# Performance work log

Hardware: AMD Instinct MI355X
Metric: run time of the kernel (lower is better)

The kernel has to match this reference:

```python
import jax, jax.numpy as jnp
import numpy as np

VOCAB = 32000
WORDVEC = 256
HIDDEN = 512
NULL_TOKEN = 0


def setup_inputs() -> dict:
    key = jax.random.key(0)
    ks = jax.random.split(key, 8)
    N, Tp1 = 16, 257
    captions = jax.random.randint(ks[0], (N, Tp1), 0, VOCAB, dtype=jnp.int64 if jax.config.jax_enable_x64 else jnp.int32)
    W_embed = jax.random.normal(ks[1], (VOCAB, WORDVEC), jnp.float32) / 100.0
    Wx = jax.random.normal(ks[2], (WORDVEC, 4 * HIDDEN), jnp.float32) / np.sqrt(WORDVEC).astype(np.float32)
    Wh = jax.random.normal(ks[3], (HIDDEN, 4 * HIDDEN), jnp.float32) / np.sqrt(HIDDEN).astype(np.float32)
    b = jnp.zeros((4 * HIDDEN,), jnp.float32)
    W_vocab = jax.random.normal(ks[4], (HIDDEN, VOCAB), jnp.float32) / np.sqrt(HIDDEN).astype(np.float32)
    b_vocab = jnp.zeros((VOCAB,), jnp.float32)
    h_init = jax.random.normal(ks[5], (HIDDEN,), jnp.float32)
    return {"captions": captions, "W_embed": W_embed, "Wx": Wx, "Wh": Wh,
            "b": b, "W_vocab": W_vocab, "b_vocab": b_vocab, "h_init": h_init}


def reference(captions, W_embed, Wx, Wh, b, W_vocab, b_vocab, h_init):
    cap_in = captions[:, :-1]   # [N, T]
    cap_out = captions[:, 1:]   # [N, T]
    mask = (cap_out != NULL_TOKEN).astype(jnp.float32)
    N = cap_in.shape[0]
    H = h_init.shape[0]

    # Embedding lookup: [N, T, D]
    x = W_embed[cap_in]
    # Precompute input projections as one big GEMM: [T, N, 4H]
    xw = jnp.einsum('ntd,dk->tnk', x, Wx) + b

    h0 = jnp.tile(h_init, (N, 1))          # [N, H]
    c0 = jnp.zeros_like(h0)                 # lstm_forward starts c at zeros

    def step(carry, a_x):
        h, c = carry
        a = a_x + h @ Wh                    # [N, 4H]
        i, f, o, g = jnp.split(a, 4, axis=-1)
        i = jax.nn.sigmoid(i)
        f = jax.nn.sigmoid(f)
        o = jax.nn.sigmoid(o)
        g = jnp.tanh(g)
        c = f * c + i * g
        h = o * jnp.tanh(c)
        return (h, c), h

    _, hs = jax.lax.scan(step, (h0, c0), xw)  # hs: [T, N, H]

    # Temporal affine: [N, T, V]
    logits = jnp.einsum('tnh,hv->ntv', hs, W_vocab) + b_vocab
    logp = jax.nn.log_softmax(logits, axis=-1)
    nll = -jnp.take_along_axis(logp, cap_out[..., None], axis=-1)[..., 0]
    loss = jnp.sum(nll * mask) / N
    return loss
```

## Files before the change

### kernel.cpp

```cpp
#include <hip/hip_runtime.h>

#define VOCAB   32000
#define WORDVEC 256
#define HIDDEN  512
#define TSTEPS  256
#define NBATCH  16
#define NROWS   (TSTEPS*NBATCH)
#define GATES   (4*HIDDEN)
#define NVB     125
#define NWG     32
#define NVBLK   8000
#define SPINCAP (1<<16)

typedef __attribute__((ext_vector_type(8))) short short8;
typedef __attribute__((ext_vector_type(4))) float f32x4;
typedef unsigned long long u64;

#define AGLOAD(p) __hip_atomic_load((p), __ATOMIC_RELAXED, __HIP_MEMORY_SCOPE_AGENT)

__device__ __forceinline__ unsigned short f2bf(float x){
    union { float f; unsigned int u; } v; v.f = x;
    unsigned int r = v.u + 0x7fffu + ((v.u >> 16) & 1u);
    return (unsigned short)(r >> 16);
}

__global__ __launch_bounds__(256) void prep_all(const int* __restrict__ captions,
        const float* __restrict__ Wemb, const float* __restrict__ Wx,
        const float* __restrict__ b, float* __restrict__ xw,
        const float* __restrict__ Wh, unsigned short* __restrict__ Whp,
        const float* __restrict__ h_init, u64* __restrict__ hx,
        const float* __restrict__ Wv, unsigned short* __restrict__ WvP,
        int* __restrict__ prog){
    __shared__ float s[64][65];
    float (*xs)[WORDVEC] = (float(*)[WORDVEC])s;
    __shared__ int toks[8];
    int bid = blockIdx.x;
    int tid = threadIdx.x;
    if (bid < 512){
        int r0 = bid * 8;
        if (tid < 8){
            int r = r0 + tid; int t = r >> 4, n = r & 15;
            toks[tid] = captions[n*257 + t];
        }
        __syncthreads();
        for (int i = 0; i < 8; ++i){
            int lin = tid + i*256;
            int ri = lin >> 8, d = lin & 255;
            xs[ri][d] = Wemb[(long)toks[ri]*WORDVEC + d];
        }
        __syncthreads();
        float4 b0 = *(const float4*)(b + tid*4);
        float4 b1 = *(const float4*)(b + 1024 + tid*4);
        float acc[8][8];
        for (int ri = 0; ri < 8; ++ri){
            acc[ri][0]=b0.x; acc[ri][1]=b0.y; acc[ri][2]=b0.z; acc[ri][3]=b0.w;
            acc[ri][4]=b1.x; acc[ri][5]=b1.y; acc[ri][6]=b1.z; acc[ri][7]=b1.w;
        }
        for (int d = 0; d < WORDVEC; ++d){
            float4 w0 = *(const float4*)(Wx + (long)d*GATES + tid*4);
            float4 w1 = *(const float4*)(Wx + (long)d*GATES + 1024 + tid*4);
            #pragma unroll
            for (int ri = 0; ri < 8; ++ri){
                float xv = xs[ri][d];
                acc[ri][0] += xv*w0.x; acc[ri][1] += xv*w0.y;
                acc[ri][2] += xv*w0.z; acc[ri][3] += xv*w0.w;
                acc[ri][4] += xv*w1.x; acc[ri][5] += xv*w1.y;
                acc[ri][6] += xv*w1.z; acc[ri][7] += xv*w1.w;
            }
        }
        for (int ri = 0; ri < 8; ++ri){
            float4 o0 = {acc[ri][0],acc[ri][1],acc[ri][2],acc[ri][3]};
            float4 o1 = {acc[ri][4],acc[ri][5],acc[ri][6],acc[ri][7]};
            *(float4*)(xw + (long)(r0+ri)*GATES + tid*4) = o0;
            *(float4*)(xw + (long)(r0+ri)*GATES + 1024 + tid*4) = o1;
        }
    } else if (bid < 544){
        int w = bid - 512;
        for (int item = tid; item < 4096; item += 256){
            int f = item >> 6;
            int L = item & 63;
            int kt = f >> 2, nt = f & 3;
            int q = L >> 4, ln = L & 15;
            int col = nt*HIDDEN + w*16 + ln;
            short8 vvec;
            for (int jj = 0; jj < 8; ++jj){
                int k = kt*32 + q*8 + jj;
                vvec[jj] = (short)f2bf(Wh[(long)k*GATES + col]);
            }
            *(short8*)(Whp + ((long)w*4096 + item)*8) = vvec;
        }
    } else if (bid < 560){
        if (bid == 544 && tid < 32) prog[tid] = 0;
        int p = (bid - 544)*256 + tid;
        int fq = p >> 6;
        int j  = (p & 3) * 2;
        int u0 = (fq>>2)*32 + (fq&3)*8 + j;
        u64 pk = (u64)f2bf(h_init[u0]) | ((u64)f2bf(h_init[u0+1]) << 16);
        hx[p] = pk;
    } else {
        int tile = bid - 560;
        int v0 = (tile >> 3) * 64;
        int k0 = (tile & 7) * 64;
        for (int i = 0; i < 16; ++i){
            int lin = tid + i*256;
            int kk = lin >> 6, vv = lin & 63;
            s[kk][vv] = Wv[(long)(k0+kk)*VOCAB + v0 + vv];
        }
        __syncthreads();
        for (int i = 0; i < 2; ++i){
            int lr = tid + i*256;
            int f  = lr >> 6;
            int vbl = f >> 1, ktl = f & 1;
            int L = lr & 63, q = L >> 4, ln = L & 15;
            short8 o;
            #pragma unroll
            for (int j = 0; j < 8; ++j)
                o[j] = (short)f2bf(s[ktl*32 + q*8 + j][vbl*16 + ln]);
            long vb = (long)(tile >> 3)*4 + vbl;
            long kt = (long)(tile & 7)*2 + ktl;
            *(short8*)(WvP + ((vb*16 + kt)*64 + L)*8) = o;
        }
    }
}

__global__ __launch_bounds__(256, 2) void lstm_vocab(const float* __restrict__ xw,
        const unsigned short* __restrict__ Whp, u64* __restrict__ hx,
        unsigned short* __restrict__ hsP, int* __restrict__ prog,
        const unsigned short* __restrict__ WvP, const float* __restrict__ bvoc,
        const int* __restrict__ captions, float* __restrict__ pmax,
        float* __restrict__ psum, float* __restrict__ tlog){
    __shared__ unsigned int hstage[4096];
    __shared__ float a_s[4][16][16];
    __shared__ int   tgt_s[64];
    __shared__ float wmax_s[4][64], wsum_s[4][64];
    int tid = threadIdx.x;

    if (blockIdx.x >= NWG){
        int vid = blockIdx.x - NWG;
        int pri = vid / 2000;
        int idx = vid % 2000;
        int bn  = idx % 125;
        int bm  = (idx / 125) * 4 + pri;
        int need = (pri + 1) * 4;

        if (tid == 0){
            int cnt = 0;
            for (;;){
                int mn = 1 << 30;
                for (int i = 0; i < 32; ++i){
                    int p = AGLOAD(&prog[i]);
                    mn = p < mn ? p : mn;
                }
                if (mn >= need) break;
                __builtin_amdgcn_s_sleep(32);
                if (++cnt > SPINCAP) break;
            }
        }
        __syncthreads();

        int wv = tid >> 6, L = tid & 63;
        int q = L >> 4, ln = L & 15;
        if (tid < 64){
            int rg = bm*64 + tid;
            tgt_s[tid] = captions[(rg >> 8)*257 + (rg & 255) + 1];
        }
        __syncthreads();
        f32x4 acc[4][4];
        for (int mt=0;mt<4;++mt) for (int nt=0;nt<4;++nt) acc[mt][nt] = (f32x4){0.f,0.f,0.f,0.f};
        int colb = bn*256 + wv*64;
        const unsigned short* aB = hsP + ((long)(bm*4)*16)*512;
        const unsigned short* bB = WvP + ((long)(bn*16 + wv*4)*16)*512;
        #pragma unroll 4
        for (int kt = 0; kt < 16; ++kt){
            short8 a[4], bb[4];
            #pragma unroll
            for (int mt=0;mt<4;++mt)
                a[mt] = *(const short8*)(aB + ((long)(mt*16 + kt)*64 + L)*8);
            #pragma unroll
            for (int nt=0;nt<4;++nt)
                bb[nt] = *(const short8*)(bB + ((long)(nt*16 + kt)*64 + L)*8);
            #pragma unroll
            for (int mt=0;mt<4;++mt)
                #pragma unroll
                for (int nt=0;nt<4;++nt)
                    acc[mt][nt] = __builtin_amdgcn_mfma_f32_16x16x32_bf16(a[mt], bb[nt], acc[mt][nt], 0,0,0);
        }
        float bv[4];
        #pragma unroll
        for (int nt=0;nt<4;++nt) bv[nt] = bvoc[colb + nt*16 + ln];
        #pragma unroll
        for (int mt=0;mt<4;++mt) for (int nt=0;nt<4;++nt) for (int r=0;r<4;++r)
            acc[mt][nt][r] += bv[nt];
        #pragma unroll
        for (int mt=0;mt<4;++mt) for (int r=0;r<4;++r){
            int rl = mt*16 + q*4 + r;
            int tg = tgt_s[rl] - colb;
            if (tg >= 0 && tg < 64){
                int nt = tg >> 4;
                if ((tg & 15) == ln) tlog[bm*64 + rl] = acc[mt][nt][r];
            }
        }
        #pragma unroll
        for (int mt=0;mt<4;++mt){
            #pragma unroll
            for (int r=0;r<4;++r){
                float m = fmaxf(fmaxf(acc[mt][0][r],acc[mt][1][r]), fmaxf(acc[mt][2][r],acc[mt][3][r]));
                for (int d=1; d<16; d<<=1) m = fmaxf(m, __shfl_xor(m, d, 16));
                float s = __expf(acc[mt][0][r]-m) + __expf(acc[mt][1][r]-m)
                        + __expf(acc[mt][2][r]-m) + __expf(acc[mt][3][r]-m);
                for (int d=1; d<16; d<<=1) s += __shfl_xor(s, d, 16);
                if (ln == 0){ int rl = mt*16 + q*4 + r; wmax_s[wv][rl] = m; wsum_s[wv][rl] = s; }
            }
        }
        __syncthreads();
        if (tid < 64){
            float M = fmaxf(fmaxf(wmax_s[0][tid],wmax_s[1][tid]), fmaxf(wmax_s[2][tid],wmax_s[3][tid]));
            float S = 0.f;
            for (int ww=0; ww<4; ++ww) S += wsum_s[ww][tid]*__expf(wmax_s[ww][tid]-M);
            pmax[(long)bn*NROWS + bm*64 + tid] = M;
            psum[(long)bn*NROWS + bm*64 + tid] = S;
        }
        return;
    }

    int w = blockIdx.x;
    int wv = tid >> 6;
    int L = tid & 63;
    int q = L >> 4, ln = L & 15;
    int s_idx = tid >> 4, jl = tid & 15;

    short8 bw[16];
    #pragma unroll
    for (int kt = 0; kt < 16; ++kt)
        bw[kt] = *(const short8*)(Whp + ((long)w*4096 + (kt*4+wv)*64 + L)*8);

    float c_r = 0.f;
    int fq_pub = (w>>1)*4 + (w&1)*2 + (jl>>3);
    int pubIdx = fq_pub*64 + s_idx*4 + ((jl>>1)&3);
    int kt_h = w >> 1;
    int q_h  = ((w & 1) << 1) | (jl >> 3);
    int j_h  = jl & 7;
    unsigned int* hsP32 = (unsigned int*)hsP;

    for (int t = 0; t < TSTEPS; ++t){
        long xb = (long)(t*16 + s_idx)*GATES + w*16 + jl;
        float xg0 = xw[xb], xg1 = xw[xb+512], xg2 = xw[xb+1024], xg3 = xw[xb+1536];

        const u64* hr = hx + (t & 1)*4096;
        u64*       hw = hx + ((t+1) & 1)*4096;

        u64 v[16];
        #pragma unroll
        for (int i = 0; i < 16; ++i)
            v[i] = AGLOAD(hr + tid + i*256);
        for (;;){
            u64 bad = 0;
            #pragma unroll
            for (int i = 0; i < 16; ++i) bad |= (v[i] >> 32) ^ (u64)(unsigned)t;
            if (!bad) break;
            #pragma unroll
            for (int i = 0; i < 16; ++i)
                v[i] = AGLOAD(hr + tid + i*256);
        }
        #pragma unroll
        for (int i = 0; i < 16; ++i) hstage[tid + i*256] = (unsigned)v[i];
        __syncthreads();

        f32x4 acc = {0.f,0.f,0.f,0.f};
        #pragma unroll
        for (int kt = 0; kt < 16; ++kt){
            short8 a = *(const short8*)((const unsigned short*)hstage + (kt*256 + q*64 + ln*4)*2);
            acc = __builtin_amdgcn_mfma_f32_16x16x32_bf16(a, bw[kt], acc, 0, 0, 0);
        }
        #pragma unroll
        for (int r = 0; r < 4; ++r) a_s[wv][q*4 + r][ln] = acc[r];
        __syncthreads();

        float ai = a_s[0][s_idx][jl] + xg0;
        float af = a_s[1][s_idx][jl] + xg1;
        float ao = a_s[2][s_idx][jl] + xg2;
        float ag = a_s[3][s_idx][jl] + xg3;
        float ig = 1.f/(1.f + __expf(-ai));
        float fg = 1.f/(1.f + __expf(-af));
        float og = 1.f/(1.f + __expf(-ao));
        float gg = 2.f/(1.f + __expf(-2.f*ag)) - 1.f;
        c_r = fg*c_r + ig*gg;
        float hv = og * (2.f/(1.f + __expf(-2.f*c_r)) - 1.f);
        unsigned short hb = f2bf(hv);

        int hv32 = (int)hb;
        int other = __shfl(hv32, L ^ 1);
        int rb = s_idx*16 + (t >> 4);
        if ((jl & 1) == 0){
            u64 pk = (u64)(unsigned short)hv32
                   | ((u64)(unsigned short)other << 16)
                   | ((u64)(unsigned)(t+1) << 32);
            __hip_atomic_store(hw + pubIdx, pk, __ATOMIC_RELAXED, __HIP_MEMORY_SCOPE_AGENT);
            unsigned int hp = (unsigned int)(unsigned short)hv32
                            | ((unsigned int)(unsigned short)other << 16);
            __hip_atomic_store(hsP32 + (((long)(rb*16 + kt_h))*64 + q_h*16 + (t & 15))*4 + (j_h >> 1),
                               hp, __ATOMIC_RELAXED, __HIP_MEMORY_SCOPE_AGENT);
        }
        if ((t & 15) == 15){
            asm volatile("s_waitcnt vmcnt(0)" ::: "memory");
            __syncthreads();
            if (tid == 0)
                __hip_atomic_store(&prog[w], (t >> 4) + 1, __ATOMIC_RELAXED, __HIP_MEMORY_SCOPE_AGENT);
        }
    }
}

__global__ __launch_bounds__(256) void reduce_loss(const float* __restrict__ pmax,
        const float* __restrict__ psum, const float* __restrict__ tlog,
        const int* __restrict__ captions, float* __restrict__ out){
    int r = blockIdx.x*256 + threadIdx.x;
    float M = -1e30f;
    for (int p=0;p<NVB;++p) M = fmaxf(M, pmax[(long)p*NROWS + r]);
    float S = 0.f;
    for (int p=0;p<NVB;++p) S += psum[(long)p*NROWS + r]*__expf(pmax[(long)p*NROWS + r]-M);
    float lse = M + logf(S);
    float nll = lse - tlog[r];
    int tok = captions[(r >> 8)*257 + (r & 255) + 1];
    float val = (tok != 0) ? nll : 0.f;
    __shared__ float red[256];
    red[threadIdx.x] = val; __syncthreads();
    for (int s=128; s>0; s>>=1){
        if (threadIdx.x < s) red[threadIdx.x] += red[threadIdx.x+s];
        __syncthreads();
    }
    if (threadIdx.x == 0) atomicAdd(out, red[0] * (1.0f/16.0f));
}

extern "C" void kernel_launch(void* const* d_in, const int* in_sizes, int n_in,
                              void* d_out, int out_size, void* d_ws, size_t ws_size,
                              hipStream_t stream){
    const int*   captions = (const int*)  d_in[0];
    const float* Wemb     = (const float*)d_in[1];
    const float* Wx       = (const float*)d_in[2];
    const float* Wh       = (const float*)d_in[3];
    const float* b        = (const float*)d_in[4];
    const float* Wv       = (const float*)d_in[5];
    const float* bvoc     = (const float*)d_in[6];
    const float* h_init   = (const float*)d_in[7];

    char* ws = (char*)d_ws;
    float*          xw   = (float*)         (ws + 0);
    unsigned short* WvP  = (unsigned short*)(ws + 33554432);
    unsigned short* hsP  = (unsigned short*)(ws + 66322432);
    float*          pmax = (float*)         (ws + 70516736);
    float*          psum = (float*)         (ws + 72564736);
    float*          tlog = (float*)         (ws + 74612736);
    unsigned short* Whp  = (unsigned short*)(ws + 74629120);
    u64*            hx   = (u64*)           (ws + 76726272);
    int*            prog = (int*)           (ws + 76791808);

    float* out_f = (float*)d_out;

    (void)hipMemsetAsync(d_out, 0, sizeof(float), stream);

    hipLaunchKernelGGL(prep_all,    dim3(4560),       dim3(256), 0, stream,
                       captions, Wemb, Wx, b, xw, Wh, Whp, h_init, hx, Wv, WvP, prog);
    hipLaunchKernelGGL(lstm_vocab,  dim3(NWG+NVBLK),  dim3(256), 0, stream,
                       xw, Whp, hx, hsP, prog, WvP, bvoc, captions, pmax, psum, tlog);
    hipLaunchKernelGGL(reduce_loss, dim3(16),         dim3(256), 0, stream,
                       pmax, psum, tlog, captions, out_f);
}
```

Measured before the change: 1.169 ms.

## Restructure vocab GEMM inner loop for register pressure and remap tile order

The vocab-projection blocks now run a non-unrolled k loop that loads A/B fragments in staged groups, separated by scheduling barriers, and reloads two B fragments instead of holding all eight in registers. This lowers register pressure and removes the min-2-waves launch bound. Block-to-tile mapping is also permuted so consecutive blocks cover different column/row tiles, changing L2 reuse of W_vocab. The cost is extra global loads per k step and a new scheduling order that may expose latency.

```diff
diff --git a/kernel.cpp b/kernel.cpp
--- a/kernel.cpp
+++ b/kernel.cpp
@@ -17,6 +17,7 @@
 typedef unsigned long long u64;
 
 #define AGLOAD(p) __hip_atomic_load((p), __ATOMIC_RELAXED, __HIP_MEMORY_SCOPE_AGENT)
+#define MFMA16(a,b,c) __builtin_amdgcn_mfma_f32_16x16x32_bf16((a),(b),(c),0,0,0)
 
 __device__ __forceinline__ unsigned short f2bf(float x){
     union { float f; unsigned int u; } v; v.f = x;
@@ -123,7 +124,7 @@
     }
 }
 
-__global__ __launch_bounds__(256, 2) void lstm_vocab(const float* __restrict__ xw,
+__global__ __launch_bounds__(256) void lstm_vocab(const float* __restrict__ xw,
         const unsigned short* __restrict__ Whp, u64* __restrict__ hx,
         unsigned short* __restrict__ hsP, int* __restrict__ prog,
         const unsigned short* __restrict__ WvP, const float* __restrict__ bvoc,
@@ -139,8 +140,9 @@
         int vid = blockIdx.x - NWG;
         int pri = vid / 2000;
         int idx = vid % 2000;
-        int bn  = idx % 125;
-        int bm  = (idx / 125) * 4 + pri;
+        int p   = (idx & 7)*250 + (idx >> 3);
+        int bn  = p >> 4;
+        int bm  = (p & 15)*4 + pri;
         int need = (pri + 1) * 4;
 
         if (tid == 0){
@@ -148,8 +150,8 @@
             for (;;){
                 int mn = 1 << 30;
                 for (int i = 0; i < 32; ++i){
-                    int p = AGLOAD(&prog[i]);
-                    mn = p < mn ? p : mn;
+                    int pv = AGLOAD(&prog[i]);
+                    mn = pv < mn ? pv : mn;
                 }
                 if (mn >= need) break;
                 __builtin_amdgcn_s_sleep(32);
@@ -168,22 +170,31 @@
         f32x4 acc[4][4];
         for (int mt=0;mt<4;++mt) for (int nt=0;nt<4;++nt) acc[mt][nt] = (f32x4){0.f,0.f,0.f,0.f};
         int colb = bn*256 + wv*64;
-        const unsigned short* aB = hsP + ((long)(bm*4)*16)*512;
-        const unsigned short* bB = WvP + ((long)(bn*16 + wv*4)*16)*512;
-        #pragma unroll 4
+        const unsigned short* aB = hsP + ((long)(bm*4)*16)*512 + (long)L*8;
+        const unsigned short* bB = WvP + ((long)(bn*16 + wv*4)*16)*512 + (long)L*8;
+        #pragma unroll 1
         for (int kt = 0; kt < 16; ++kt){
-            short8 a[4], bb[4];
-            #pragma unroll
-            for (int mt=0;mt<4;++mt)
-                a[mt] = *(const short8*)(aB + ((long)(mt*16 + kt)*64 + L)*8);
-            #pragma unroll
-            for (int nt=0;nt<4;++nt)
-                bb[nt] = *(const short8*)(bB + ((long)(nt*16 + kt)*64 + L)*8);
-            #pragma unroll
-            for (int mt=0;mt<4;++mt)
-                #pragma unroll
-                for (int nt=0;nt<4;++nt)
-                    acc[mt][nt] = __builtin_amdgcn_mfma_f32_16x16x32_bf16(a[mt], bb[nt], acc[mt][nt], 0,0,0);
+            const short8* aK = (const short8*)(aB + (long)kt*512);
+            const short8* bK = (const short8*)(bB + (long)kt*512);
+            short8 a0 = aK[0],    a1 = aK[1024];
+            short8 b0 = bK[0],    b1 = bK[1024];
+            acc[0][0] = MFMA16(a0,b0,acc[0][0]); acc[0][1] = MFMA16(a0,b1,acc[0][1]);
+            acc[1][0] = MFMA16(a1,b0,acc[1][0]); acc[1][1] = MFMA16(a1,b1,acc[1][1]);
+            __builtin_amdgcn_sched_barrier(0);
+            short8 b2 = bK[2048], b3 = bK[3072];
+            acc[0][2] = MFMA16(a0,b2,acc[0][2]); acc[0][3] = MFMA16(a0,b3,acc[0][3]);
+            acc[1][2] = MFMA16(a1,b2,acc[1][2]); acc[1][3] = MFMA16(a1,b3,acc[1][3]);
+            __builtin_amdgcn_sched_barrier(0);
+            short8 a2 = aK[2048], a3 = aK[3072];
+            acc[2][2] = MFMA16(a2,b2,acc[2][2]); acc[2][3] = MFMA16(a2,b3,acc[2][3]);
+            acc[3][2] = MFMA16(a3,b2,acc[3][2]); acc[3][3] = MFMA16(a3,b3,acc[3][3]);
+            __builtin_amdgcn_sched_barrier(0);
+            u64 bKo = (u64)bK; asm volatile("" : "+v"(bKo));
+            const short8* bK2 = (const short8*)bKo;
+            short8 c0 = bK2[0], c1 = bK2[1024];
+            acc[2][0] = MFMA16(a2,c0,acc[2][0]); acc[2][1] = MFMA16(a2,c1,acc[2][1]);
+            acc[3][0] = MFMA16(a3,c0,acc[3][0]); acc[3][1] = MFMA16(a3,c1,acc[3][1]);
+            __builtin_amdgcn_sched_barrier(0);
         }
         float bv[4];
         #pragma unroll
@@ -270,7 +281,7 @@
         #pragma unroll
         for (int kt = 0; kt < 16; ++kt){
             short8 a = *(const short8*)((const unsigned short*)hstage + (kt*256 + q*64 + ln*4)*2);
-            acc = __builtin_amdgcn_mfma_f32_16x16x32_bf16(a, bw[kt], acc, 0, 0, 0);
+            acc = MFMA16(a, bw[kt], acc);
         }
         #pragma unroll
         for (int r = 0; r < 4; ++r) a_s[wv][q*4 + r][ln] = acc[r];
```

Measured after the change: 1.047 ms. 10.4% less time.
